# Performance work log

Hardware: AMD Instinct MI355X
Metric: run time of the kernel (lower is better)

Reference implementation:

```python
import jax, jax.numpy as jnp
import numpy as np

N, E, B, F, H = 400000, 1600000, 8192, 64, 96


def gcn_conv(x, src, dst, W, b, n):
    # PyG GCNConv: x' = D^-1/2 (A+I) D^-1/2 (x W) + b
    x = x @ W
    loop = jnp.arange(n)
    s = jnp.concatenate([src, loop])
    d = jnp.concatenate([dst, loop])
    deg = jax.ops.segment_sum(jnp.ones_like(d, x.dtype), d, num_segments=n)
    dinv = jnp.where(deg > 0, jax.lax.rsqrt(deg), 0.0)
    norm = dinv[s] * dinv[d]  # [E+N]
    return jax.ops.segment_sum(norm[:, None] * x[s], d, num_segments=n) + b


def forward_convs(x, src, dst, Ws, bs, n):
    for i in range(len(Ws)):
        x = gcn_conv(x, src, dst, Ws[i], bs[i], n)
        if i < len(Ws) - 1:
            x = jax.nn.relu(x)
    return x


def att_pool(x, batch, W1, b1, W2, b2, nb):
    # GlobalAttention: gate = Lin(F,F)->ReLU->Lin(F,1); segment softmax; weighted sum
    g = (jax.nn.relu(x @ W1 + b1) @ W2 + b2)[:, 0]  # [N]
    gmax = jax.ops.segment_max(g, batch, num_segments=nb)
    e = jnp.exp(g - gmax[batch])
    denom = jax.ops.segment_sum(e, batch, num_segments=nb)
    a = e / denom[batch]
    return jax.ops.segment_sum(a[:, None] * x, batch, num_segments=nb)


def mean_pool(x, batch, nb):
    s = jax.ops.segment_sum(x, batch, num_segments=nb)
    cnt = jax.ops.segment_sum(jnp.ones_like(batch, x.dtype), batch, num_segments=nb)
    return s / jnp.maximum(cnt, 1.0)[:, None]


def setup_inputs() -> dict:
    key = jax.random.key(0)
    ks = jax.random.split(key, 32)
    inp = {
        "x_p": jax.random.normal(ks[0], (N, F), jnp.float32),
        "x_d": jax.random.normal(ks[1], (N, F), jnp.float32),
        "edge_attr_p": jax.random.normal(ks[2], (E, 8), jnp.float32),
        "edge_attr_d": jax.random.normal(ks[3], (E, 8), jnp.float32),
        "edge_index_p": jax.random.randint(ks[4], (2, E), 0, N),
        "edge_index_d": jax.random.randint(ks[5], (2, E), 0, N),
        "x_p_batch": jnp.sort(jax.random.randint(ks[6], (N,), 0, B)),
        "x_d_batch": jnp.sort(jax.random.randint(ks[7], (N,), 0, B)),
    }
    def lin(k, fi, fo):
        bnd = 1.0 / np.sqrt(fi)
        k1, k2 = jax.random.split(k)
        return (jax.random.uniform(k1, (fi, fo), jnp.float32, -bnd, bnd),
                jax.random.uniform(k2, (fo,), jnp.float32, -bnd, bnd))
    inp["gate_W1"], inp["gate_b1"] = lin(ks[8], F, F)
    inp["gate_W2"], inp["gate_b2"] = lin(ks[9], F, 1)
    dims = [(F, H), (H, H), (H, H)]
    for side, base in (("p", 10), ("d", 13)):
        for i, (fi, fo) in enumerate(dims):
            W, b = lin(ks[base + i], fi, fo)
            inp[f"conv{side}_W{i}"], inp[f"conv{side}_b{i}"] = W, b
    inp["lin_W0"], inp["lin_b0"] = lin(ks[16], 2 * H + 2 * F, H)
    inp["lin_W1"], inp["lin_b1"] = lin(ks[17], H, 1)
    return inp


def reference(x_p, x_d, edge_attr_p, edge_attr_d, edge_index_p, edge_index_d,
              x_p_batch, x_d_batch, gate_W1, gate_b1, gate_W2, gate_b2,
              convp_W0, convp_b0, convp_W1, convp_b1, convp_W2, convp_b2,
              convd_W0, convd_b0, convd_W1, convd_b1, convd_W2, convd_b2,
              lin_W0, lin_b0, lin_W1, lin_b1):
    n, nb = x_p.shape[0], B
    xp_att = att_pool(x_p, x_p_batch, gate_W1, gate_b1, gate_W2, gate_b2, nb)
    xd_att = att_pool(x_d, x_d_batch, gate_W1, gate_b1, gate_W2, gate_b2, nb)
    xp = forward_convs(x_p, edge_index_p[0], edge_index_p[1],
                       [convp_W0, convp_W1, convp_W2], [convp_b0, convp_b1, convp_b2], n)
    xd = forward_convs(x_d, edge_index_d[0], edge_index_d[1],
                       [convd_W0, convd_W1, convd_W2], [convd_b0, convd_b1, convd_b2], n)
    xp = mean_pool(xp, x_p_batch, nb)
    xd = mean_pool(xd, x_d_batch, nb)
    x = jnp.concatenate([xp, xd, xp_att, xd_att], axis=1)  # [B, 2H+2F]
    # dropout p=0.5 is identity in eval mode
    x = jax.nn.relu(x @ lin_W0 + lin_b0)
    return x @ lin_W1 + lin_b1  # [B, 1]
```

## Files before the change

### kernel.cpp

```cpp
#include <hip/hip_runtime.h>

#define NN 400000
#define EE 1600000
#define NB 8192

typedef float vf4 __attribute__((ext_vector_type(4)));
typedef float vf2 __attribute__((ext_vector_type(2)));

__global__ void k_seg(const int* __restrict__ batch, int* __restrict__ start){
  int b = blockIdx.x*256 + threadIdx.x;
  if (b > NB) return;
  int lo = 0, hi = NN;
  while (lo < hi){ int mid = (lo+hi)>>1; if (batch[mid] < b) lo = mid+1; else hi = mid; }
  start[b] = lo;
}

__global__ __launch_bounds__(256) void k_gate(const float* __restrict__ x,
    const float* __restrict__ W1, const float* __restrict__ b1,
    const float* __restrict__ W2, const float* __restrict__ b2,
    float* __restrict__ g){
  __shared__ __align__(16) float sX[64*68];
  __shared__ __align__(16) float sW[64*64];
  __shared__ float sB[128];
  __shared__ float sRed[64*17];
  const int tid = threadIdx.x;
  const int r0 = blockIdx.x << 6;
  for (int i = tid; i < 4096; i += 256) sW[i] = W1[i];
  if (tid < 64) sB[tid] = b1[tid];
  else if (tid < 128) sB[tid] = W2[tid-64];
  for (int i = tid; i < 4096; i += 256){
    int r = i >> 6, k = i & 63;
    sX[k*68 + r] = x[(size_t)r0*64 + i];
  }
  __syncthreads();
  const int tx = tid & 15;
  const int ty = tid >> 4;
  float acc[4][4];
  #pragma unroll
  for (int i = 0; i < 4; ++i)
    #pragma unroll
    for (int j = 0; j < 4; ++j) acc[i][j] = 0.f;
  for (int k = 0; k < 64; ++k){
    vf4 a = *(const vf4*)&sX[k*68 + ty*4];
    vf4 w = *(const vf4*)&sW[k*64 + tx*4];
    #pragma unroll
    for (int i = 0; i < 4; ++i)
      #pragma unroll
      for (int j = 0; j < 4; ++j)
        acc[i][j] = fmaf(a[i], w[j], acc[i][j]);
  }
  #pragma unroll
  for (int i = 0; i < 4; ++i){
    float p = 0.f;
    #pragma unroll
    for (int j = 0; j < 4; ++j){
      int c = tx*4 + j;
      p = fmaf(fmaxf(acc[i][j] + sB[c], 0.f), sB[64+c], p);
    }
    sRed[(ty*4+i)*17 + tx] = p;
  }
  __syncthreads();
  if (tid < 64){
    float s = 0.f;
    #pragma unroll
    for (int j = 0; j < 16; ++j) s += sRed[tid*17 + j];
    g[r0 + tid] = s + b2[0];
  }
}

__global__ __launch_bounds__(64) void k_att(const float* __restrict__ x, const float* __restrict__ g,
    const int* __restrict__ start, float* __restrict__ att){
  int b = blockIdx.x, lane = threadIdx.x;
  int s0 = start[b], s1 = start[b+1];
  if (s1 <= s0){ att[b*64+lane] = 0.f; return; }
  float m = -3.0e38f;
  for (int i = s0+lane; i < s1; i += 64) m = fmaxf(m, g[i]);
  #pragma unroll
  for (int off = 32; off; off >>= 1) m = fmaxf(m, __shfl_xor(m, off));
  float s = 0.f;
  for (int i = s0+lane; i < s1; i += 64) s += expf(g[i]-m);
  #pragma unroll
  for (int off = 32; off; off >>= 1) s += __shfl_xor(s, off);
  float acc = 0.f;
  for (int i = s0; i < s1; ++i)
    acc = fmaf(expf(g[i]-m), x[(size_t)i*64+lane], acc);
  att[b*64+lane] = acc / s;
}

__global__ void k_zero(int* __restrict__ degI, int* __restrict__ gc){
  int i = blockIdx.x*256 + threadIdx.x;
  if (i < NN) degI[i] = 0;
  if (i == 0) *gc = 0;
}
__global__ void k_count(const int* __restrict__ dst, int* __restrict__ degI){
  int e = blockIdx.x*256 + threadIdx.x;
  if (e < EE) atomicAdd(&degI[dst[e]], 1);
}
__global__ __launch_bounds__(256) void k_alloc(const int* __restrict__ degI, int* __restrict__ gc,
    int* __restrict__ base, int* __restrict__ cursor, float* __restrict__ dinv){
  int i = blockIdx.x*256 + threadIdx.x;
  int lane = threadIdx.x & 63;
  int d = (i < NN) ? degI[i] : 0;
  int incl = d;
  #pragma unroll
  for (int off = 1; off < 64; off <<= 1){
    int t = __shfl_up(incl, off);
    if (lane >= off) incl += t;
  }
  int waveTotal = __shfl(incl, 63);
  int wbase = 0;
  if (lane == 63) wbase = atomicAdd(gc, waveTotal);
  wbase = __shfl(wbase, 63);
  if (i < NN){
    int b = wbase + incl - d;
    base[i] = b; cursor[i] = b;
    dinv[i] = 1.f / sqrtf((float)d + 1.f);
  }
}
__global__ void k_fillcsr(const int* __restrict__ src, const int* __restrict__ dst,
                          const float* __restrict__ dinv,
                          int* __restrict__ cursor, int2* __restrict__ csr2){
  int e = blockIdx.x*256 + threadIdx.x;
  if (e >= EE) return;
  int s = src[e];
  int p = atomicAdd(&cursor[dst[e]], 1);
  csr2[p] = make_int2(s, __float_as_int(dinv[s]));
}

template<int K, bool RELU>
__global__ __launch_bounds__(256) void k_gemm(const float* __restrict__ in,
    const float* __restrict__ W, const float* __restrict__ bias, float* __restrict__ out){
  __shared__ __align__(16) float sIn[K*68];
  __shared__ __align__(16) float sW[K*96];
  __shared__ float sB[96];
  const int tid = threadIdx.x;
  const int r0 = blockIdx.x << 6;
  for (int i = tid; i < K*96; i += 256) sW[i] = W[i];
  if (tid < 96) sB[tid] = bias[tid];
  for (int i = tid; i < 64*K; i += 256){
    int r = i / K, k = i - r*K;
    sIn[k*68 + r] = in[(size_t)r0*K + i];
  }
  __syncthreads();
  const int tx = tid & 15;
  const int ty = tid >> 4;
  float acc[4][6];
  #pragma unroll
  for (int i = 0; i < 4; ++i)
    #pragma unroll
    for (int j = 0; j < 6; ++j) acc[i][j] = 0.f;
  for (int k = 0; k < K; ++k){
    vf4 a   = *(const vf4*)&sIn[k*68 + ty*4];
    vf2 w01 = *(const vf2*)&sW[k*96 + tx*6];
    vf2 w23 = *(const vf2*)&sW[k*96 + tx*6 + 2];
    vf2 w45 = *(const vf2*)&sW[k*96 + tx*6 + 4];
    float w[6] = {w01[0], w01[1], w23[0], w23[1], w45[0], w45[1]};
    #pragma unroll
    for (int i = 0; i < 4; ++i)
      #pragma unroll
      for (int j = 0; j < 6; ++j)
        acc[i][j] = fmaf(a[i], w[j], acc[i][j]);
  }
  #pragma unroll
  for (int i = 0; i < 4; ++i){
    size_t row = r0 + ty*4 + i;
    #pragma unroll
    for (int j = 0; j < 6; ++j){
      float v = acc[i][j] + sB[tx*6 + j];
      if (RELU) v = fmaxf(v, 0.f);
      out[row*96 + tx*6 + j] = v;
    }
  }
}

__global__ __launch_bounds__(256) void k_gather96(const float* __restrict__ xw,
    const int2* __restrict__ csr2, const int* __restrict__ base, const int* __restrict__ degI,
    const float* __restrict__ dinv, float* __restrict__ out){
  const int grp  = threadIdx.x >> 5;
  const int lane = threadIdx.x & 31;
  const int i = (blockIdx.x << 3) + grp;
  const bool act = lane < 24;
  const vf4* __restrict__ xw4 = (const vf4*)xw;
  const float di = dinv[i];
  const int b0 = base[i], cnt = degI[i];
  vf4 s = {0.f,0.f,0.f,0.f};
  if (act) s = di * xw4[(size_t)i*24 + lane];
  int t = 0;
  for (; t+4 <= cnt; t += 4){
    int2 e0 = csr2[b0+t], e1 = csr2[b0+t+1], e2 = csr2[b0+t+2], e3 = csr2[b0+t+3];
    if (act){
      vf4 v0 = xw4[(size_t)e0.x*24 + lane];
      vf4 v1 = xw4[(size_t)e1.x*24 + lane];
      vf4 v2 = xw4[(size_t)e2.x*24 + lane];
      vf4 v3 = xw4[(size_t)e3.x*24 + lane];
      s += __int_as_float(e0.y)*v0;
      s += __int_as_float(e1.y)*v1;
      s += __int_as_float(e2.y)*v2;
      s += __int_as_float(e3.y)*v3;
    }
  }
  for (; t < cnt; ++t){
    int2 e = csr2[b0+t];
    if (act){
      vf4 v = xw4[(size_t)e.x*24 + lane];
      s += __int_as_float(e.y)*v;
    }
  }
  if (act){
    vf4 r = di * s;
    ((vf4*)out)[(size_t)i*24 + lane] = r;
  }
}

__global__ __launch_bounds__(256) void k_gather64(const float* __restrict__ x,
    const int2* __restrict__ csr2, const int* __restrict__ base, const int* __restrict__ degI,
    const float* __restrict__ dinv, float* __restrict__ out){
  const int grp  = threadIdx.x >> 4;
  const int lane = threadIdx.x & 15;
  const int i = (blockIdx.x << 4) + grp;
  const vf4* __restrict__ x4 = (const vf4*)x;
  const float di = dinv[i];
  const int b0 = base[i], cnt = degI[i];
  vf4 s = di * x4[(size_t)i*16 + lane];
  int t = 0;
  for (; t+4 <= cnt; t += 4){
    int2 e0 = csr2[b0+t], e1 = csr2[b0+t+1], e2 = csr2[b0+t+2], e3 = csr2[b0+t+3];
    vf4 v0 = x4[(size_t)e0.x*16 + lane];
    vf4 v1 = x4[(size_t)e1.x*16 + lane];
    vf4 v2 = x4[(size_t)e2.x*16 + lane];
    vf4 v3 = x4[(size_t)e3.x*16 + lane];
    s += __int_as_float(e0.y)*v0;
    s += __int_as_float(e1.y)*v1;
    s += __int_as_float(e2.y)*v2;
    s += __int_as_float(e3.y)*v3;
  }
  for (; t < cnt; ++t){
    int2 e = csr2[b0+t];
    vf4 v = x4[(size_t)e.x*16 + lane];
    s += __int_as_float(e.y)*v;
  }
  vf4 r = di * s;
  ((vf4*)out)[(size_t)i*16 + lane] = r;
}

__global__ __launch_bounds__(128) void k_mean(const float* __restrict__ h,
    const int* __restrict__ start, float* __restrict__ mean){
  int b = blockIdx.x, f = threadIdx.x;
  if (f >= 96) return;
  int s0 = start[b], s1 = start[b+1];
  float acc = 0.f;
  for (int i = s0; i < s1; ++i) acc += h[(size_t)i*96+f];
  mean[b*96+f] = acc / fmaxf((float)(s1-s0), 1.f);
}

__global__ __launch_bounds__(128) void k_final(const float* __restrict__ meanP, const float* __restrict__ meanD,
    const float* __restrict__ attP, const float* __restrict__ attD,
    const float* __restrict__ W0, const float* __restrict__ b0,
    const float* __restrict__ W1, const float* __restrict__ b1,
    float* __restrict__ out){
  __shared__ float cat[320];
  __shared__ float hb[96];
  int b = blockIdx.x, tid = threadIdx.x;
  if (tid < 96){ cat[tid] = meanP[b*96+tid]; cat[96+tid] = meanD[b*96+tid]; }
  if (tid < 64){ cat[192+tid] = attP[b*64+tid]; cat[256+tid] = attD[b*64+tid]; }
  __syncthreads();
  if (tid < 96){
    float acc = b0[tid];
    for (int k = 0; k < 320; ++k) acc = fmaf(cat[k], W0[k*96+tid], acc);
    hb[tid] = fmaxf(acc, 0.f) * W1[tid];
  }
  __syncthreads();
  if (tid == 0){
    float y = b1[0];
    for (int j = 0; j < 96; ++j) y += hb[j];
    out[b] = y;
  }
}

extern "C" void kernel_launch(void* const* d_in, const int* in_sizes, int n_in,
                              void* d_out, int out_size, void* d_ws, size_t ws_size,
                              hipStream_t stream){
  const float* x_p = (const float*)d_in[0];
  const float* x_d = (const float*)d_in[1];
  const int* ei_p = (const int*)d_in[4];
  const int* ei_d = (const int*)d_in[5];
  const int* batch_p = (const int*)d_in[6];
  const int* batch_d = (const int*)d_in[7];
  const float* gW1 = (const float*)d_in[8];
  const float* gb1 = (const float*)d_in[9];
  const float* gW2 = (const float*)d_in[10];
  const float* gb2 = (const float*)d_in[11];
  const float* cW[2][3] = {{(const float*)d_in[12],(const float*)d_in[14],(const float*)d_in[16]},
                           {(const float*)d_in[18],(const float*)d_in[20],(const float*)d_in[22]}};
  const float* cB[2][3] = {{(const float*)d_in[13],(const float*)d_in[15],(const float*)d_in[17]},
                           {(const float*)d_in[19],(const float*)d_in[21],(const float*)d_in[23]}};
  const float* lW0 = (const float*)d_in[24];
  const float* lb0 = (const float*)d_in[25];
  const float* lW1 = (const float*)d_in[26];
  const float* lb1 = (const float*)d_in[27];
  float* out = (float*)d_out;

  float* fws = (float*)d_ws;
  size_t off = 0;
  float* A     = fws + off; off += (size_t)NN*96;
  float* Bf    = fws + off; off += (size_t)NN*96;
  float* dinv  = fws + off; off += NN;
  float* g     = fws + off; off += NN;
  float* attP  = fws + off; off += (size_t)NB*64;
  float* attD  = fws + off; off += (size_t)NB*64;
  float* meanP = fws + off; off += (size_t)NB*96;
  float* meanD = fws + off; off += (size_t)NB*96;
  int2* csr2  = (int2*)(fws + off);
  int* iws = (int*)(csr2 + EE);
  int* segP   = iws;             iws += NB+1;
  int* segD   = iws;             iws += NB+1;
  int* degI   = iws;             iws += NN;
  int* base   = iws;             iws += NN;
  int* cursor = iws;             iws += NN;
  int* gc     = iws;             iws += 1;

  k_seg<<<(NB+1+255)/256, 256, 0, stream>>>(batch_p, segP);
  k_seg<<<(NB+1+255)/256, 256, 0, stream>>>(batch_d, segD);

  for (int side = 0; side < 2; ++side){
    const float* x  = side ? x_d : x_p;
    const int* src = side ? ei_d : ei_p;
    const int* dst = src + EE;
    const int* seg = side ? segD : segP;
    float* att  = side ? attD : attP;
    float* mean = side ? meanD : meanP;

    k_gate<<<NN/64, 256, 0, stream>>>(x, gW1, gb1, gW2, gb2, g);
    k_att<<<NB, 64, 0, stream>>>(x, g, seg, att);

    k_zero   <<<(NN+255)/256, 256, 0, stream>>>(degI, gc);
    k_count  <<<(EE+255)/256, 256, 0, stream>>>(dst, degI);
    k_alloc  <<<(NN+255)/256, 256, 0, stream>>>(degI, gc, base, cursor, dinv);
    k_fillcsr<<<(EE+255)/256, 256, 0, stream>>>(src, dst, dinv, cursor, csr2);

    k_gather64<<<NN/16, 256, 0, stream>>>(x, csr2, base, degI, dinv, A);
    k_gemm<64,true ><<<NN/64, 256, 0, stream>>>(A, cW[side][0], cB[side][0], Bf);
    k_gather96<<<NN/8, 256, 0, stream>>>(Bf, csr2, base, degI, dinv, A);
    k_gemm<96,true ><<<NN/64, 256, 0, stream>>>(A, cW[side][1], cB[side][1], Bf);
    k_gather96<<<NN/8, 256, 0, stream>>>(Bf, csr2, base, degI, dinv, A);
    k_gemm<96,false><<<NN/64, 256, 0, stream>>>(A, cW[side][2], cB[side][2], Bf);

    k_mean<<<NB, 128, 0, stream>>>(Bf, seg, mean);
  }
  k_final<<<NB, 128, 0, stream>>>(meanP, meanD, attP, attD, lW0, lb0, lW1, lb1, out);
}
```

Before: 2.509 ms.

## Split neighbor gathers into two feature-half passes for cache locality

Each SpMM gather kernel is split into two launches, each covering half of the feature columns (32 of 64 or 48 of 96), with the per-node thread group halved. The working set of gathered rows per pass is halved, so the randomly accessed feature matrix is meant to fit better in L2/LLC. The cost is reading the CSR index and weight arrays twice, an extra launch per gather, and smaller 128- or 192-byte segments per gathered row. In the 96-feature kernel, 4 of every 16 lanes now sit idle instead of 8 of every 32.

```diff
diff --git a/kernel.cpp b/kernel.cpp
--- a/kernel.cpp
+++ b/kernel.cpp
@@ -173,26 +173,27 @@
   }
 }
 
-__global__ __launch_bounds__(256) void k_gather96(const float* __restrict__ xw,
+template<int PASS>
+__global__ __launch_bounds__(256) void k_gather96s(const float* __restrict__ xw,
     const int2* __restrict__ csr2, const int* __restrict__ base, const int* __restrict__ degI,
     const float* __restrict__ dinv, float* __restrict__ out){
-  const int grp  = threadIdx.x >> 5;
-  const int lane = threadIdx.x & 31;
-  const int i = (blockIdx.x << 3) + grp;
-  const bool act = lane < 24;
+  const int grp  = threadIdx.x >> 4;
+  const int lane = threadIdx.x & 15;
+  const int i = (blockIdx.x << 4) + grp;
+  const bool act = lane < 12;
   const vf4* __restrict__ xw4 = (const vf4*)xw;
   const float di = dinv[i];
   const int b0 = base[i], cnt = degI[i];
   vf4 s = {0.f,0.f,0.f,0.f};
-  if (act) s = di * xw4[(size_t)i*24 + lane];
+  if (act) s = di * xw4[(size_t)i*24 + PASS*12 + lane];
   int t = 0;
   for (; t+4 <= cnt; t += 4){
     int2 e0 = csr2[b0+t], e1 = csr2[b0+t+1], e2 = csr2[b0+t+2], e3 = csr2[b0+t+3];
     if (act){
-      vf4 v0 = xw4[(size_t)e0.x*24 + lane];
-      vf4 v1 = xw4[(size_t)e1.x*24 + lane];
-      vf4 v2 = xw4[(size_t)e2.x*24 + lane];
-      vf4 v3 = xw4[(size_t)e3.x*24 + lane];
+      vf4 v0 = xw4[(size_t)e0.x*24 + PASS*12 + lane];
+      vf4 v1 = xw4[(size_t)e1.x*24 + PASS*12 + lane];
+      vf4 v2 = xw4[(size_t)e2.x*24 + PASS*12 + lane];
+      vf4 v3 = xw4[(size_t)e3.x*24 + PASS*12 + lane];
       s += __int_as_float(e0.y)*v0;
       s += __int_as_float(e1.y)*v1;
       s += __int_as_float(e2.y)*v2;
@@ -202,33 +203,34 @@
   for (; t < cnt; ++t){
     int2 e = csr2[b0+t];
     if (act){
-      vf4 v = xw4[(size_t)e.x*24 + lane];
+      vf4 v = xw4[(size_t)e.x*24 + PASS*12 + lane];
       s += __int_as_float(e.y)*v;
     }
   }
   if (act){
     vf4 r = di * s;
-    ((vf4*)out)[(size_t)i*24 + lane] = r;
-  }
-}
-
-__global__ __launch_bounds__(256) void k_gather64(const float* __restrict__ x,
+    ((vf4*)out)[(size_t)i*24 + PASS*12 + lane] = r;
+  }
+}
+
+template<int PASS>
+__global__ __launch_bounds__(256) void k_gather64s(const float* __restrict__ x,
     const int2* __restrict__ csr2, const int* __restrict__ base, const int* __restrict__ degI,
     const float* __restrict__ dinv, float* __restrict__ out){
-  const int grp  = threadIdx.x >> 4;
-  const int lane = threadIdx.x & 15;
-  const int i = (blockIdx.x << 4) + grp;
+  const int grp  = threadIdx.x >> 3;
+  const int lane = threadIdx.x & 7;
+  const int i = (blockIdx.x << 5) + grp;
   const vf4* __restrict__ x4 = (const vf4*)x;
   const float di = dinv[i];
   const int b0 = base[i], cnt = degI[i];
-  vf4 s = di * x4[(size_t)i*16 + lane];
+  vf4 s = di * x4[(size_t)i*16 + PASS*8 + lane];
   int t = 0;
   for (; t+4 <= cnt; t += 4){
     int2 e0 = csr2[b0+t], e1 = csr2[b0+t+1], e2 = csr2[b0+t+2], e3 = csr2[b0+t+3];
-    vf4 v0 = x4[(size_t)e0.x*16 + lane];
-    vf4 v1 = x4[(size_t)e1.x*16 + lane];
-    vf4 v2 = x4[(size_t)e2.x*16 + lane];
-    vf4 v3 = x4[(size_t)e3.x*16 + lane];
+    vf4 v0 = x4[(size_t)e0.x*16 + PASS*8 + lane];
+    vf4 v1 = x4[(size_t)e1.x*16 + PASS*8 + lane];
+    vf4 v2 = x4[(size_t)e2.x*16 + PASS*8 + lane];
+    vf4 v3 = x4[(size_t)e3.x*16 + PASS*8 + lane];
     s += __int_as_float(e0.y)*v0;
     s += __int_as_float(e1.y)*v1;
     s += __int_as_float(e2.y)*v2;
@@ -236,11 +238,11 @@
   }
   for (; t < cnt; ++t){
     int2 e = csr2[b0+t];
-    vf4 v = x4[(size_t)e.x*16 + lane];
+    vf4 v = x4[(size_t)e.x*16 + PASS*8 + lane];
     s += __int_as_float(e.y)*v;
   }
   vf4 r = di * s;
-  ((vf4*)out)[(size_t)i*16 + lane] = r;
+  ((vf4*)out)[(size_t)i*16 + PASS*8 + lane] = r;
 }
 
 __global__ __launch_bounds__(128) void k_mean(const float* __restrict__ h,
@@ -338,11 +340,14 @@
     k_alloc  <<<(NN+255)/256, 256, 0, stream>>>(degI, gc, base, cursor, dinv);
     k_fillcsr<<<(EE+255)/256, 256, 0, stream>>>(src, dst, dinv, cursor, csr2);
 
-    k_gather64<<<NN/16, 256, 0, stream>>>(x, csr2, base, degI, dinv, A);
+    k_gather64s<0><<<NN/32, 256, 0, stream>>>(x, csr2, base, degI, dinv, A);
+    k_gather64s<1><<<NN/32, 256, 0, stream>>>(x, csr2, base, degI, dinv, A);
     k_gemm<64,true ><<<NN/64, 256, 0, stream>>>(A, cW[side][0], cB[side][0], Bf);
-    k_gather96<<<NN/8, 256, 0, stream>>>(Bf, csr2, base, degI, dinv, A);
+    k_gather96s<0><<<NN/16, 256, 0, stream>>>(Bf, csr2, base, degI, dinv, A);
+    k_gather96s<1><<<NN/16, 256, 0, stream>>>(Bf, csr2, base, degI, dinv, A);
     k_gemm<96,true ><<<NN/64, 256, 0, stream>>>(A, cW[side][1], cB[side][1], Bf);
-    k_gather96<<<NN/8, 256, 0, stream>>>(Bf, csr2, base, degI, dinv, A);
+    k_gather96s<0><<<NN/16, 256, 0, stream>>>(Bf, csr2, base, degI, dinv, A);
+    k_gather96s<1><<<NN/16, 256, 0, stream>>>(Bf, csr2, base, degI, dinv, A);
     k_gemm<96,false><<<NN/64, 256, 0, stream>>>(A, cW[side][2], cB[side][2], Bf);
 
     k_mean<<<NB, 128, 0, stream>>>(Bf, seg, mean);
```

New measurement: 2.670 ms. +6.4%, slower.
